# Performance work log

Measured on AMD Instinct MI355X. Metric: run time of the kernel, lower is better.

The kernel has to match this reference:

```python
import jax, jax.numpy as jnp
import numpy as np

BIG = 1e4  # larger than any image dimension; safe in fp32 when squared


def _edt(e):
    # e: [H, W] binary float mask. Exact Euclidean distance transform:
    # distance from each nonzero pixel to the nearest zero pixel
    # (matches cv2.distanceTransform(e, cv2.DIST_L2, maskSize=0)).
    H, W = e.shape
    zero = e == 0
    x = jnp.arange(W, dtype=jnp.float32)[None, :]            # [1, W]
    # 1D pass along rows: distance (in x) to nearest zero in the same row
    last = jax.lax.cummax(jnp.where(zero, x, -BIG), axis=1)              # nearest zero to the left
    nxt = -jax.lax.cummax(jnp.where(zero, -x, -BIG), axis=1, reverse=True)  # nearest zero to the right
    g = jnp.minimum(x - last, nxt - x)                        # [H, W], BIG-ish if row has no zero
    g2 = jnp.minimum(g, BIG) ** 2                             # squared row distance
    # 2D pass along columns: dist2[y, x] = min_r g2[r, x] + (y - r)^2 (exact EDT)
    y = jnp.arange(H, dtype=jnp.float32)
    d2 = (y[:, None] - y[None, :]) ** 2                       # [H, H]
    dist2 = jnp.min(g2[None, :, :] + d2[:, :, None], axis=1)  # [H, W]
    return jnp.sqrt(dist2)


def _min_max_norm(d):
    lo, hi = d.min(), d.max()
    return (d - lo) / (hi - lo + 1e-8)


def _edge_weight(edge):
    # edge: [B, 1, H, W] binary float
    e = edge[:, 0]  # [B, H, W]
    # lax.map keeps peak memory to one [H,H,W] candidate tensor at a time
    w = jax.lax.map(lambda ei: _min_max_norm(_edt(ei)), e)
    return w[:, None]  # [B, 1, H, W]


def setup_inputs() -> dict:
    key = jax.random.key(0)
    k1, k2, k3, k4 = jax.random.split(key, 4)
    shape = (16, 1, 384, 384)
    eps = 1e-4
    pred = jax.random.uniform(k1, shape, jnp.float32, eps, 1.0 - eps)
    pred_edge = jax.random.uniform(k2, shape, jnp.float32, eps, 1.0 - eps)
    label = jax.random.randint(k3, shape, 0, 2).astype(jnp.float32)
    edge = jax.random.randint(k4, shape, 0, 2).astype(jnp.float32)
    return {"pred": pred, "pred_edge": pred_edge, "label": label, "edge": edge}


def reference(pred, pred_edge, label, edge):
    Wm = _edge_weight(edge)  # [B, 1, H, W] in [0, 1]
    label_loss = jnp.mean(
        -(label * jnp.log(pred) + (1.0 - label) * jnp.log(1.0 - pred)) * (1.0 + Wm)
    )
    edge_loss = jnp.mean(
        -(edge * jnp.log(pred_edge) + (1.0 - edge) * jnp.log(1.0 - pred_edge))
    )
    return label_loss + edge_loss
```

## Files before the change

### kernel.cpp

```cpp
#include <hip/hip_runtime.h>

typedef unsigned long long u64;
typedef unsigned int u32;

#define NIMG 16
#define H 384
#define W 384
#define NPIX (H*W)
#define NTOT (NIMG*NPIX)
#define FBIG 10000.0f

#define RPB 96
#define NRB 4
#define NCT 12
#define EBLOCKS (NCT*NRB*NIMG)
#define NROW (NIMG*H)

__device__ __forceinline__ float bflo(u32 w){ return __uint_as_float(w<<16); }
__device__ __forceinline__ float bfhi(u32 w){ return __uint_as_float(w & 0xFFFF0000u); }

__device__ __forceinline__ void detect_flag(const u32* lw, int tid, u32* sflag) {
    if (tid < 64) {
        u32 a = 0;
        #pragma unroll
        for (int k = 0; k < 4; ++k) a |= lw[(tid & 63)*4 + k] & 0xFFFFu;
        u64 b = __ballot(a != 0u);
        if (tid == 0) *sflag = (b != 0ull) ? 1u : 0u;
    }
}

__global__ __launch_bounds__(256) void rowscan_kernel(
        const void* __restrict__ e, const u32* __restrict__ label_u32,
        float* __restrict__ g2, u32* __restrict__ mn, u32* __restrict__ mx) {
    __shared__ u32 sflag;
    int tid = threadIdx.x;
    if (blockIdx.x == 0 && tid < NIMG) { mn[tid] = 0x7f800000u; mx[tid] = 0u; }
    detect_flag(label_u32, tid, &sflag);
    __syncthreads();
    bool isb = (sflag != 0u);

    int lane = tid & 63;
    int row  = blockIdx.x * 4 + (tid >> 6);

    u64 zm[6];
    if (isb) {
        const unsigned short* er = (const unsigned short*)e + (size_t)row * W;
        #pragma unroll
        for (int t = 0; t < 6; ++t) zm[t] = __ballot(er[t*64 + lane] == 0);
    } else {
        const float* er = (const float*)e + (size_t)row * W;
        #pragma unroll
        for (int t = 0; t < 6; ++t) zm[t] = __ballot(er[t*64 + lane] == 0.0f);
    }

    float* gr = g2 + (size_t)row * W;
    #pragma unroll
    for (int t = 0; t < 6; ++t) {
        int c = t*64 + lane;
        u64 m = zm[t] & ((lane == 63) ? ~0ull : ((1ull << (lane+1)) - 1ull));
        int tt = t;
        while (m == 0ull && tt > 0) m = zm[--tt];
        float dl = m ? (float)(c - (tt*64 + 63 - __builtin_clzll(m)))
                     : ((float)c + FBIG);
        m = zm[t] & ((lane == 0) ? ~0ull : ~((1ull << lane) - 1ull));
        tt = t;
        while (m == 0ull && tt < 5) m = zm[++tt];
        float dr = m ? (float)((tt*64 + __builtin_ctzll(m)) - c)
                     : (FBIG - (float)c);
        float g = fminf(fminf(dl, dr), FBIG);
        gr[c] = g * g;
    }
}

__global__ __launch_bounds__(256) void edt_loss_kernel(
    const float* __restrict__ g2,
    const void* __restrict__ pred, const void* __restrict__ pred_edge,
    const void* __restrict__ label, const void* __restrict__ edge,
    u32* __restrict__ mn, u32* __restrict__ mx,
    float* __restrict__ partials) {

    __shared__ u32 sflag;
    __shared__ float cr[4][5];

    int tid = threadIdx.x;
    int img = blockIdx.z;
    int c0  = blockIdx.x * 32;
    int r0  = blockIdx.y * RPB;

    detect_flag((const u32*)label, tid, &sflag);
    __syncthreads();

    const float* g2i = g2 + (size_t)img * NPIX;
    int c2t = tid & 7;
    int rg  = tid >> 3;
    int rb  = r0 + rg;
    const float* gcol = g2i + c0 + c2t * 4;

    float4 best[3];
    float ub = 0.0f;
    #pragma unroll
    for (int i = 0; i < 3; ++i) {
        best[i] = *(const float4*)(gcol + (rb + 32*i) * W);
        ub = fmaxf(ub, fmaxf(fmaxf(best[i].x, best[i].y), fmaxf(best[i].z, best[i].w)));
    }
    #pragma unroll
    for (int off = 1; off < 64; off <<= 1)
        ub = fmaxf(ub, __shfl_xor(ub, off));
    int jcap = (int)ceilf(sqrtf(ub)) + 1;
    if (jcap > H - 1) jcap = H - 1;

    for (int j = 1; j <= jcap; ++j) {
        float jj = (float)(j * j);
        #pragma unroll
        for (int i = 0; i < 3; ++i) {
            int r  = rb + 32*i;
            int ru = r - j; ru = (ru < 0) ? 0 : ru;
            int rd = r + j; rd = (rd > H-1) ? H-1 : rd;
            float4 vu = *(const float4*)(gcol + ru * W);
            float4 vd = *(const float4*)(gcol + rd * W);
            best[i].x = fminf(best[i].x, fminf(vu.x, vd.x) + jj);
            best[i].y = fminf(best[i].y, fminf(vu.y, vd.y) + jj);
            best[i].z = fminf(best[i].z, fminf(vu.z, vd.z) + jj);
            best[i].w = fminf(best[i].w, fminf(vu.w, vd.w) + jj);
        }
    }

    bool isb = (sflag != 0u);
    float sl = 0.0f, sd = 0.0f, se = 0.0f;
    float tmin = 3.0e38f, tmax = 0.0f;
    #pragma unroll
    for (int i = 0; i < 3; ++i) {
        float dv[4];
        dv[0] = sqrtf(best[i].x); dv[1] = sqrtf(best[i].y);
        dv[2] = sqrtf(best[i].z); dv[3] = sqrtf(best[i].w);
        #pragma unroll
        for (int cc = 0; cc < 4; ++cc) {
            tmin = fminf(tmin, dv[cc]);
            tmax = fmaxf(tmax, dv[cc]);
        }
        int r = rb + 32*i;
        size_t base = (size_t)img * NPIX + (size_t)r * W + c0 + c2t * 4;
        float p[4], q[4], lv[4], ev[4];
        if (isb) {
            uint2 up = *(const uint2*)((const unsigned short*)pred      + base);
            uint2 uq = *(const uint2*)((const unsigned short*)pred_edge + base);
            uint2 ul = *(const uint2*)((const unsigned short*)label     + base);
            uint2 ue = *(const uint2*)((const unsigned short*)edge      + base);
            p[0]=bflo(up.x); p[1]=bfhi(up.x); p[2]=bflo(up.y); p[3]=bfhi(up.y);
            q[0]=bflo(uq.x); q[1]=bfhi(uq.x); q[2]=bflo(uq.y); q[3]=bfhi(uq.y);
            lv[0]=bflo(ul.x); lv[1]=bfhi(ul.x); lv[2]=bflo(ul.y); lv[3]=bfhi(ul.y);
            ev[0]=bflo(ue.x); ev[1]=bfhi(ue.x); ev[2]=bflo(ue.y); ev[3]=bfhi(ue.y);
        } else {
            float4 a = *(const float4*)((const float*)pred      + base);
            float4 b = *(const float4*)((const float*)pred_edge + base);
            float4 c = *(const float4*)((const float*)label     + base);
            float4 e = *(const float4*)((const float*)edge      + base);
            p[0]=a.x; p[1]=a.y; p[2]=a.z; p[3]=a.w;
            q[0]=b.x; q[1]=b.y; q[2]=b.z; q[3]=b.w;
            lv[0]=c.x; lv[1]=c.y; lv[2]=c.z; lv[3]=c.w;
            ev[0]=e.x; ev[1]=e.y; ev[2]=e.z; ev[3]=e.w;
        }
        #pragma unroll
        for (int cc = 0; cc < 4; ++cc) {
            float bl = -__logf((lv[cc] != 0.0f) ? p[cc] : 1.0f - p[cc]);
            sl += bl;
            sd = fmaf(bl, dv[cc], sd);
            se += -__logf((ev[cc] != 0.0f) ? q[cc] : 1.0f - q[cc]);
        }
    }

    #pragma unroll
    for (int off = 1; off < 64; off <<= 1) {
        sl += __shfl_xor(sl, off);
        sd += __shfl_xor(sd, off);
        se += __shfl_xor(se, off);
        tmin = fminf(tmin, __shfl_xor(tmin, off));
        tmax = fmaxf(tmax, __shfl_xor(tmax, off));
    }
    int wv = tid >> 6;
    if ((tid & 63) == 0) {
        cr[wv][0] = sl; cr[wv][1] = sd; cr[wv][2] = se;
        cr[wv][3] = tmin; cr[wv][4] = tmax;
    }
    __syncthreads();
    if (tid == 0) {
        float S1 = cr[0][0] + cr[1][0] + cr[2][0] + cr[3][0];
        float S2 = cr[0][1] + cr[1][1] + cr[2][1] + cr[3][1];
        float Se = cr[0][2] + cr[1][2] + cr[2][2] + cr[3][2];
        float Tm = fminf(fminf(cr[0][3], cr[1][3]), fminf(cr[2][3], cr[3][3]));
        float TM = fmaxf(fmaxf(cr[0][4], cr[1][4]), fmaxf(cr[2][4], cr[3][4]));
        int blk = (img * NRB + blockIdx.y) * NCT + blockIdx.x;
        partials[blk*4 + 0] = S1;
        partials[blk*4 + 1] = S2;
        partials[blk*4 + 2] = Se;
        atomicMin(&mn[img], __float_as_uint(Tm));
        atomicMax(&mx[img], __float_as_uint(TM));
    }
}

__global__ void final_kernel(const float* __restrict__ partials,
                             const u32* __restrict__ mn,
                             const u32* __restrict__ mx,
                             u32* __restrict__ out) {
    __shared__ float a1[256], a2[256], a3[256];
    __shared__ float ci[NIMG], sei[NIMG];
    int tid = threadIdx.x;
    int img = tid >> 4, s = tid & 15;
    float S1 = 0.0f, S2 = 0.0f, Se = 0.0f;
    #pragma unroll
    for (int k = 0; k < 3; ++k) {
        const float* pp = partials + (img * 48 + s + 16*k) * 4;
        S1 += pp[0]; S2 += pp[1]; Se += pp[2];
    }
    a1[tid] = S1; a2[tid] = S2; a3[tid] = Se;
    __syncthreads();
    for (int st = 8; st > 0; st >>= 1) {
        if ((tid & 15) < st) {
            a1[tid] += a1[tid+st]; a2[tid] += a2[tid+st]; a3[tid] += a3[tid+st];
        }
        __syncthreads();
    }
    if ((tid & 15) == 0) {
        float lo = __uint_as_float(mn[img]);
        float hi = __uint_as_float(mx[img]);
        float inv = 1.0f / (hi - lo + 1e-8f);
        ci[img]  = a1[tid] + (a2[tid] - lo * a1[tid]) * inv;
        sei[img] = a3[tid];
    }
    __syncthreads();
    if (tid == 0) {
        float t = 0.0f;
        for (int i = 0; i < NIMG; ++i) t += ci[i] + sei[i];
        float v = t / (float)NTOT;
        u32 fv = __float_as_uint(v);
        u32 b  = (fv + 0x7FFFu + ((fv >> 16) & 1u)) >> 16;
        out[0] = (fv & 0xFFFF0000u) | (b & 0xFFFFu);
    }
}

extern "C" void kernel_launch(void* const* d_in, const int* in_sizes, int n_in,
                              void* d_out, int out_size, void* d_ws, size_t ws_size,
                              hipStream_t stream) {
    float* ws = (float*)d_ws;
    float* g2 = ws;
    u32* mn = (u32*)(ws + NTOT);
    u32* mx = mn + 16;
    float* partials = (float*)(mx + 16);

    rowscan_kernel<<<NROW / 4, 256, 0, stream>>>(d_in[3], (const u32*)d_in[2],
                                                 g2, mn, mx);
    edt_loss_kernel<<<dim3(NCT, NRB, NIMG), 256, 0, stream>>>(
        g2, d_in[0], d_in[1], d_in[2], d_in[3], mn, mx, partials);
    final_kernel<<<1, 256, 0, stream>>>(partials, mn, mx, (u32*)d_out);
}
```

Baseline: 33.49 us.

## Fuse row scan into EDT kernel using shared-memory column tile with halo rows

Removes the separate row-scan kernel and its global g2 buffer. Each EDT block now builds the squared row distances for its 32-column strip directly into a shared tile, first for its own rows and then for only the halo rows needed given the block-wide search bound. The column min-plus pass then reads from LDS instead of global memory, and per-image min/max goes into the partials array instead of global atomics. The cost is redundant ballot work, since each row's edge mask is rescanned by all 12 column blocks, plus 48KB of LDS per block, which may limit occupancy.

```diff
diff --git a/kernel.cpp b/kernel.cpp
--- a/kernel.cpp
+++ b/kernel.cpp
@@ -14,7 +14,6 @@
 #define NRB 4
 #define NCT 12
 #define EBLOCKS (NCT*NRB*NIMG)
-#define NROW (NIMG*H)
 
 __device__ __forceinline__ float bflo(u32 w){ return __uint_as_float(w<<16); }
 __device__ __forceinline__ float bfhi(u32 w){ return __uint_as_float(w & 0xFFFF0000u); }
@@ -29,19 +28,8 @@
     }
 }
 
-__global__ __launch_bounds__(256) void rowscan_kernel(
-        const void* __restrict__ e, const u32* __restrict__ label_u32,
-        float* __restrict__ g2, u32* __restrict__ mn, u32* __restrict__ mx) {
-    __shared__ u32 sflag;
-    int tid = threadIdx.x;
-    if (blockIdx.x == 0 && tid < NIMG) { mn[tid] = 0x7f800000u; mx[tid] = 0u; }
-    detect_flag(label_u32, tid, &sflag);
-    __syncthreads();
-    bool isb = (sflag != 0u);
-
-    int lane = tid & 63;
-    int row  = blockIdx.x * 4 + (tid >> 6);
-
+__device__ __forceinline__ void build_row(const void* e, bool isb, int row,
+                                          int lane, int c0, float* tileF) {
     u64 zm[6];
     if (isb) {
         const unsigned short* er = (const unsigned short*)e + (size_t)row * W;
@@ -52,72 +40,98 @@
         #pragma unroll
         for (int t = 0; t < 6; ++t) zm[t] = __ballot(er[t*64 + lane] == 0.0f);
     }
-
-    float* gr = g2 + (size_t)row * W;
-    #pragma unroll
-    for (int t = 0; t < 6; ++t) {
-        int c = t*64 + lane;
-        u64 m = zm[t] & ((lane == 63) ? ~0ull : ((1ull << (lane+1)) - 1ull));
-        int tt = t;
-        while (m == 0ull && tt > 0) m = zm[--tt];
-        float dl = m ? (float)(c - (tt*64 + 63 - __builtin_clzll(m)))
-                     : ((float)c + FBIG);
-        m = zm[t] & ((lane == 0) ? ~0ull : ~((1ull << lane) - 1ull));
-        tt = t;
-        while (m == 0ull && tt < 5) m = zm[++tt];
-        float dr = m ? (float)((tt*64 + __builtin_ctzll(m)) - c)
-                     : (FBIG - (float)c);
-        float g = fminf(fminf(dl, dr), FBIG);
-        gr[c] = g * g;
+    int cw = c0 >> 6;
+    u64 w = zm[0];
+    #pragma unroll
+    for (int t = 1; t < 6; ++t) if (cw == t) w = zm[t];
+    int hb = -16777216;
+    #pragma unroll
+    for (int t = 0; t < 6; ++t)
+        if (t < cw && zm[t] != 0ull) hb = t*64 + 63 - __builtin_clzll(zm[t]);
+    int la = 16777216;
+    #pragma unroll
+    for (int t = 5; t >= 0; --t)
+        if (t > cw && zm[t] != 0ull) la = t*64 + __builtin_ctzll(zm[t]);
+    if (lane < 32) {
+        int c = c0 + lane;
+        int b = c & 63;
+        u64 ml = w & ((b == 63) ? ~0ull : ((1ull << (b+1)) - 1ull));
+        u64 mr = w & (~0ull << b);
+        int li = ml ? (cw*64 + 63 - __builtin_clzll(ml)) : hb;
+        int ri = mr ? (cw*64 + __builtin_ctzll(mr)) : la;
+        float g = fminf(fminf((float)(c - li), (float)(ri - c)), FBIG);
+        tileF[row*32 + lane] = g * g;
     }
 }
 
 __global__ __launch_bounds__(256) void edt_loss_kernel(
-    const float* __restrict__ g2,
     const void* __restrict__ pred, const void* __restrict__ pred_edge,
     const void* __restrict__ label, const void* __restrict__ edge,
-    u32* __restrict__ mn, u32* __restrict__ mx,
     float* __restrict__ partials) {
 
+    __shared__ float tileF[H * 32];
     __shared__ u32 sflag;
+    __shared__ float crub[4];
     __shared__ float cr[4][5];
 
-    int tid = threadIdx.x;
-    int img = blockIdx.z;
-    int c0  = blockIdx.x * 32;
-    int r0  = blockIdx.y * RPB;
+    int tid  = threadIdx.x;
+    int img  = blockIdx.z;
+    int c0   = blockIdx.x * 32;
+    int r0   = blockIdx.y * RPB;
+    int lane = tid & 63;
+    int wv   = tid >> 6;
 
     detect_flag((const u32*)label, tid, &sflag);
     __syncthreads();
-
-    const float* g2i = g2 + (size_t)img * NPIX;
+    bool isb = (sflag != 0u);
+
+    const void* eimg = isb
+        ? (const void*)((const unsigned short*)edge + (size_t)img * NPIX)
+        : (const void*)((const float*)edge + (size_t)img * NPIX);
+
+    for (int k = 0; k < 24; ++k)
+        build_row(eimg, isb, r0 + 4*k + wv, lane, c0, tileF);
+    __syncthreads();
+
+    const float4* tile4 = (const float4*)tileF;
     int c2t = tid & 7;
     int rg  = tid >> 3;
     int rb  = r0 + rg;
-    const float* gcol = g2i + c0 + c2t * 4;
 
     float4 best[3];
     float ub = 0.0f;
     #pragma unroll
     for (int i = 0; i < 3; ++i) {
-        best[i] = *(const float4*)(gcol + (rb + 32*i) * W);
+        best[i] = tile4[(rb + 32*i)*8 + c2t];
         ub = fmaxf(ub, fmaxf(fmaxf(best[i].x, best[i].y), fmaxf(best[i].z, best[i].w)));
     }
     #pragma unroll
     for (int off = 1; off < 64; off <<= 1)
         ub = fmaxf(ub, __shfl_xor(ub, off));
-    int jcap = (int)ceilf(sqrtf(ub)) + 1;
-    if (jcap > H - 1) jcap = H - 1;
-
-    for (int j = 1; j <= jcap; ++j) {
+    if (lane == 0) crub[wv] = ub;
+    __syncthreads();
+    float ubB = fmaxf(fmaxf(crub[0], crub[1]), fmaxf(crub[2], crub[3]));
+    int jcapW = (int)ceilf(sqrtf(ub))  + 1; if (jcapW > H-1) jcapW = H-1;
+    int jcapB = (int)ceilf(sqrtf(ubB)) + 1; if (jcapB > H-1) jcapB = H-1;
+
+    int n1 = (jcapB < r0) ? jcapB : r0;
+    int n2h = H - RPB - r0;
+    int n2 = (jcapB < n2h) ? jcapB : n2h;
+    for (int k = wv; k < n1 + n2; k += 4) {
+        int r = (k < n1) ? (r0 - n1 + k) : (r0 + RPB + (k - n1));
+        build_row(eimg, isb, r, lane, c0, tileF);
+    }
+    __syncthreads();
+
+    for (int j = 1; j <= jcapW; ++j) {
         float jj = (float)(j * j);
         #pragma unroll
         for (int i = 0; i < 3; ++i) {
             int r  = rb + 32*i;
             int ru = r - j; ru = (ru < 0) ? 0 : ru;
             int rd = r + j; rd = (rd > H-1) ? H-1 : rd;
-            float4 vu = *(const float4*)(gcol + ru * W);
-            float4 vd = *(const float4*)(gcol + rd * W);
+            float4 vu = tile4[ru*8 + c2t];
+            float4 vd = tile4[rd*8 + c2t];
             best[i].x = fminf(best[i].x, fminf(vu.x, vd.x) + jj);
             best[i].y = fminf(best[i].y, fminf(vu.y, vd.y) + jj);
             best[i].z = fminf(best[i].z, fminf(vu.z, vd.z) + jj);
@@ -125,7 +139,6 @@
         }
     }
 
-    bool isb = (sflag != 0u);
     float sl = 0.0f, sd = 0.0f, se = 0.0f;
     float tmin = 3.0e38f, tmax = 0.0f;
     #pragma unroll
@@ -177,8 +190,7 @@
         tmin = fminf(tmin, __shfl_xor(tmin, off));
         tmax = fmaxf(tmax, __shfl_xor(tmax, off));
     }
-    int wv = tid >> 6;
-    if ((tid & 63) == 0) {
+    if (lane == 0) {
         cr[wv][0] = sl; cr[wv][1] = sd; cr[wv][2] = se;
         cr[wv][3] = tmin; cr[wv][4] = tmax;
     }
@@ -190,39 +202,36 @@
         float Tm = fminf(fminf(cr[0][3], cr[1][3]), fminf(cr[2][3], cr[3][3]));
         float TM = fmaxf(fmaxf(cr[0][4], cr[1][4]), fmaxf(cr[2][4], cr[3][4]));
         int blk = (img * NRB + blockIdx.y) * NCT + blockIdx.x;
-        partials[blk*4 + 0] = S1;
-        partials[blk*4 + 1] = S2;
-        partials[blk*4 + 2] = Se;
-        atomicMin(&mn[img], __float_as_uint(Tm));
-        atomicMax(&mx[img], __float_as_uint(TM));
+        float* pp = partials + blk * 5;
+        pp[0] = S1; pp[1] = S2; pp[2] = Se; pp[3] = Tm; pp[4] = TM;
     }
 }
 
 __global__ void final_kernel(const float* __restrict__ partials,
-                             const u32* __restrict__ mn,
-                             const u32* __restrict__ mx,
                              u32* __restrict__ out) {
-    __shared__ float a1[256], a2[256], a3[256];
+    __shared__ float a1[256], a2[256], a3[256], a4[256], a5[256];
     __shared__ float ci[NIMG], sei[NIMG];
     int tid = threadIdx.x;
     int img = tid >> 4, s = tid & 15;
-    float S1 = 0.0f, S2 = 0.0f, Se = 0.0f;
+    float S1 = 0.0f, S2 = 0.0f, Se = 0.0f, Tm = 3.0e38f, TM = 0.0f;
     #pragma unroll
     for (int k = 0; k < 3; ++k) {
-        const float* pp = partials + (img * 48 + s + 16*k) * 4;
+        const float* pp = partials + (img * 48 + s + 16*k) * 5;
         S1 += pp[0]; S2 += pp[1]; Se += pp[2];
-    }
-    a1[tid] = S1; a2[tid] = S2; a3[tid] = Se;
+        Tm = fminf(Tm, pp[3]); TM = fmaxf(TM, pp[4]);
+    }
+    a1[tid]=S1; a2[tid]=S2; a3[tid]=Se; a4[tid]=Tm; a5[tid]=TM;
     __syncthreads();
     for (int st = 8; st > 0; st >>= 1) {
         if ((tid & 15) < st) {
             a1[tid] += a1[tid+st]; a2[tid] += a2[tid+st]; a3[tid] += a3[tid+st];
+            a4[tid] = fminf(a4[tid], a4[tid+st]);
+            a5[tid] = fmaxf(a5[tid], a5[tid+st]);
         }
         __syncthreads();
     }
     if ((tid & 15) == 0) {
-        float lo = __uint_as_float(mn[img]);
-        float hi = __uint_as_float(mx[img]);
+        float lo = a4[tid], hi = a5[tid];
         float inv = 1.0f / (hi - lo + 1e-8f);
         ci[img]  = a1[tid] + (a2[tid] - lo * a1[tid]) * inv;
         sei[img] = a3[tid];
@@ -241,15 +250,9 @@
 extern "C" void kernel_launch(void* const* d_in, const int* in_sizes, int n_in,
                               void* d_out, int out_size, void* d_ws, size_t ws_size,
                               hipStream_t stream) {
-    float* ws = (float*)d_ws;
-    float* g2 = ws;
-    u32* mn = (u32*)(ws + NTOT);
-    u32* mx = mn + 16;
-    float* partials = (float*)(mx + 16);
-
-    rowscan_kernel<<<NROW / 4, 256, 0, stream>>>(d_in[3], (const u32*)d_in[2],
-                                                 g2, mn, mx);
+    float* partials = (float*)d_ws;
+
     edt_loss_kernel<<<dim3(NCT, NRB, NIMG), 256, 0, stream>>>(
-        g2, d_in[0], d_in[1], d_in[2], d_in[3], mn, mx, partials);
-    final_kernel<<<1, 256, 0, stream>>>(partials, mn, mx, (u32*)d_out);
-}
+        d_in[0], d_in[1], d_in[2], d_in[3], partials);
+    final_kernel<<<1, 256, 0, stream>>>(partials, (u32*)d_out);
+}
```

Result: slower. 37.29 us (+11.3%).

## Stage column strip of g2 in LDS, prefetch loss inputs, drop min/max atomics

Applied to the files above, without the earlier changes.

Each EDT block now copies the full 384x32 column strip of squared row distances into shared memory (48 KB) and runs the column min-plus search from LDS instead of global/L2. The loss inputs are prefetched into registers before the search so their latency overlaps it. Per-image min/max move from global atomics into the partials buffer and are reduced in the final kernel. The cost is that every block loads the whole strip, four times the rows it owns, and the large LDS footprint limits how many blocks fit per CU.

```diff
diff --git a/kernel.cpp b/kernel.cpp
--- a/kernel.cpp
+++ b/kernel.cpp
@@ -31,10 +31,9 @@
 
 __global__ __launch_bounds__(256) void rowscan_kernel(
         const void* __restrict__ e, const u32* __restrict__ label_u32,
-        float* __restrict__ g2, u32* __restrict__ mn, u32* __restrict__ mx) {
+        float* __restrict__ g2) {
     __shared__ u32 sflag;
     int tid = threadIdx.x;
-    if (blockIdx.x == 0 && tid < NIMG) { mn[tid] = 0x7f800000u; mx[tid] = 0u; }
     detect_flag(label_u32, tid, &sflag);
     __syncthreads();
     bool isb = (sflag != 0u);
@@ -76,31 +75,61 @@
     const float* __restrict__ g2,
     const void* __restrict__ pred, const void* __restrict__ pred_edge,
     const void* __restrict__ label, const void* __restrict__ edge,
-    u32* __restrict__ mn, u32* __restrict__ mx,
     float* __restrict__ partials) {
 
+    __shared__ float tileF[H * 32];
     __shared__ u32 sflag;
     __shared__ float cr[4][5];
 
-    int tid = threadIdx.x;
-    int img = blockIdx.z;
-    int c0  = blockIdx.x * 32;
-    int r0  = blockIdx.y * RPB;
+    int tid  = threadIdx.x;
+    int img  = blockIdx.z;
+    int c0   = blockIdx.x * 32;
+    int r0   = blockIdx.y * RPB;
+    int lane = tid & 63;
+    int wv   = tid >> 6;
 
     detect_flag((const u32*)label, tid, &sflag);
-    __syncthreads();
 
     const float* g2i = g2 + (size_t)img * NPIX;
+    float4* tile4w = (float4*)tileF;
+    #pragma unroll
+    for (int k = 0; k < 12; ++k) {
+        int gi  = tid + 256*k;
+        int row = gi >> 3, c2 = gi & 7;
+        tile4w[gi] = *(const float4*)(g2i + row * W + c0 + c2 * 4);
+    }
+    __syncthreads();
+    bool isb = (sflag != 0u);
+
+    const float4* tile4 = (const float4*)tileF;
     int c2t = tid & 7;
     int rg  = tid >> 3;
     int rb  = r0 + rg;
-    const float* gcol = g2i + c0 + c2t * 4;
+
+    uint4 st_p[3], st_q[3], st_l[3], st_e[3];
+    #pragma unroll
+    for (int i = 0; i < 3; ++i) {
+        size_t base = (size_t)img * NPIX + (size_t)(rb + 32*i) * W + c0 + c2t * 4;
+        if (isb) {
+            uint2 a = *(const uint2*)((const unsigned short*)pred      + base);
+            uint2 b = *(const uint2*)((const unsigned short*)pred_edge + base);
+            uint2 c = *(const uint2*)((const unsigned short*)label     + base);
+            uint2 d = *(const uint2*)((const unsigned short*)edge      + base);
+            st_p[i].x=a.x; st_p[i].y=a.y; st_q[i].x=b.x; st_q[i].y=b.y;
+            st_l[i].x=c.x; st_l[i].y=c.y; st_e[i].x=d.x; st_e[i].y=d.y;
+        } else {
+            st_p[i] = *(const uint4*)((const float*)pred      + base);
+            st_q[i] = *(const uint4*)((const float*)pred_edge + base);
+            st_l[i] = *(const uint4*)((const float*)label     + base);
+            st_e[i] = *(const uint4*)((const float*)edge      + base);
+        }
+    }
 
     float4 best[3];
     float ub = 0.0f;
     #pragma unroll
     for (int i = 0; i < 3; ++i) {
-        best[i] = *(const float4*)(gcol + (rb + 32*i) * W);
+        best[i] = tile4[(rb + 32*i)*8 + c2t];
         ub = fmaxf(ub, fmaxf(fmaxf(best[i].x, best[i].y), fmaxf(best[i].z, best[i].w)));
     }
     #pragma unroll
@@ -116,8 +145,8 @@
             int r  = rb + 32*i;
             int ru = r - j; ru = (ru < 0) ? 0 : ru;
             int rd = r + j; rd = (rd > H-1) ? H-1 : rd;
-            float4 vu = *(const float4*)(gcol + ru * W);
-            float4 vd = *(const float4*)(gcol + rd * W);
+            float4 vu = tile4[ru*8 + c2t];
+            float4 vd = tile4[rd*8 + c2t];
             best[i].x = fminf(best[i].x, fminf(vu.x, vd.x) + jj);
             best[i].y = fminf(best[i].y, fminf(vu.y, vd.y) + jj);
             best[i].z = fminf(best[i].z, fminf(vu.z, vd.z) + jj);
@@ -125,7 +154,6 @@
         }
     }
 
-    bool isb = (sflag != 0u);
     float sl = 0.0f, sd = 0.0f, se = 0.0f;
     float tmin = 3.0e38f, tmax = 0.0f;
     #pragma unroll
@@ -138,27 +166,21 @@
             tmin = fminf(tmin, dv[cc]);
             tmax = fmaxf(tmax, dv[cc]);
         }
-        int r = rb + 32*i;
-        size_t base = (size_t)img * NPIX + (size_t)r * W + c0 + c2t * 4;
         float p[4], q[4], lv[4], ev[4];
         if (isb) {
-            uint2 up = *(const uint2*)((const unsigned short*)pred      + base);
-            uint2 uq = *(const uint2*)((const unsigned short*)pred_edge + base);
-            uint2 ul = *(const uint2*)((const unsigned short*)label     + base);
-            uint2 ue = *(const uint2*)((const unsigned short*)edge      + base);
-            p[0]=bflo(up.x); p[1]=bfhi(up.x); p[2]=bflo(up.y); p[3]=bfhi(up.y);
-            q[0]=bflo(uq.x); q[1]=bfhi(uq.x); q[2]=bflo(uq.y); q[3]=bfhi(uq.y);
-            lv[0]=bflo(ul.x); lv[1]=bfhi(ul.x); lv[2]=bflo(ul.y); lv[3]=bfhi(ul.y);
-            ev[0]=bflo(ue.x); ev[1]=bfhi(ue.x); ev[2]=bflo(ue.y); ev[3]=bfhi(ue.y);
+            p[0]=bflo(st_p[i].x); p[1]=bfhi(st_p[i].x); p[2]=bflo(st_p[i].y); p[3]=bfhi(st_p[i].y);
+            q[0]=bflo(st_q[i].x); q[1]=bfhi(st_q[i].x); q[2]=bflo(st_q[i].y); q[3]=bfhi(st_q[i].y);
+            lv[0]=bflo(st_l[i].x); lv[1]=bfhi(st_l[i].x); lv[2]=bflo(st_l[i].y); lv[3]=bfhi(st_l[i].y);
+            ev[0]=bflo(st_e[i].x); ev[1]=bfhi(st_e[i].x); ev[2]=bflo(st_e[i].y); ev[3]=bfhi(st_e[i].y);
         } else {
-            float4 a = *(const float4*)((const float*)pred      + base);
-            float4 b = *(const float4*)((const float*)pred_edge + base);
-            float4 c = *(const float4*)((const float*)label     + base);
-            float4 e = *(const float4*)((const float*)edge      + base);
-            p[0]=a.x; p[1]=a.y; p[2]=a.z; p[3]=a.w;
-            q[0]=b.x; q[1]=b.y; q[2]=b.z; q[3]=b.w;
-            lv[0]=c.x; lv[1]=c.y; lv[2]=c.z; lv[3]=c.w;
-            ev[0]=e.x; ev[1]=e.y; ev[2]=e.z; ev[3]=e.w;
+            p[0]=__uint_as_float(st_p[i].x); p[1]=__uint_as_float(st_p[i].y);
+            p[2]=__uint_as_float(st_p[i].z); p[3]=__uint_as_float(st_p[i].w);
+            q[0]=__uint_as_float(st_q[i].x); q[1]=__uint_as_float(st_q[i].y);
+            q[2]=__uint_as_float(st_q[i].z); q[3]=__uint_as_float(st_q[i].w);
+            lv[0]=__uint_as_float(st_l[i].x); lv[1]=__uint_as_float(st_l[i].y);
+            lv[2]=__uint_as_float(st_l[i].z); lv[3]=__uint_as_float(st_l[i].w);
+            ev[0]=__uint_as_float(st_e[i].x); ev[1]=__uint_as_float(st_e[i].y);
+            ev[2]=__uint_as_float(st_e[i].z); ev[3]=__uint_as_float(st_e[i].w);
         }
         #pragma unroll
         for (int cc = 0; cc < 4; ++cc) {
@@ -177,8 +199,7 @@
         tmin = fminf(tmin, __shfl_xor(tmin, off));
         tmax = fmaxf(tmax, __shfl_xor(tmax, off));
     }
-    int wv = tid >> 6;
-    if ((tid & 63) == 0) {
+    if (lane == 0) {
         cr[wv][0] = sl; cr[wv][1] = sd; cr[wv][2] = se;
         cr[wv][3] = tmin; cr[wv][4] = tmax;
     }
@@ -190,39 +211,36 @@
         float Tm = fminf(fminf(cr[0][3], cr[1][3]), fminf(cr[2][3], cr[3][3]));
         float TM = fmaxf(fmaxf(cr[0][4], cr[1][4]), fmaxf(cr[2][4], cr[3][4]));
         int blk = (img * NRB + blockIdx.y) * NCT + blockIdx.x;
-        partials[blk*4 + 0] = S1;
-        partials[blk*4 + 1] = S2;
-        partials[blk*4 + 2] = Se;
-        atomicMin(&mn[img], __float_as_uint(Tm));
-        atomicMax(&mx[img], __float_as_uint(TM));
+        float* pp = partials + blk * 5;
+        pp[0] = S1; pp[1] = S2; pp[2] = Se; pp[3] = Tm; pp[4] = TM;
     }
 }
 
 __global__ void final_kernel(const float* __restrict__ partials,
-                             const u32* __restrict__ mn,
-                             const u32* __restrict__ mx,
                              u32* __restrict__ out) {
-    __shared__ float a1[256], a2[256], a3[256];
+    __shared__ float a1[256], a2[256], a3[256], a4[256], a5[256];
     __shared__ float ci[NIMG], sei[NIMG];
     int tid = threadIdx.x;
     int img = tid >> 4, s = tid & 15;
-    float S1 = 0.0f, S2 = 0.0f, Se = 0.0f;
+    float S1 = 0.0f, S2 = 0.0f, Se = 0.0f, Tm = 3.0e38f, TM = 0.0f;
     #pragma unroll
     for (int k = 0; k < 3; ++k) {
-        const float* pp = partials + (img * 48 + s + 16*k) * 4;
+        const float* pp = partials + (img * 48 + s + 16*k) * 5;
         S1 += pp[0]; S2 += pp[1]; Se += pp[2];
-    }
-    a1[tid] = S1; a2[tid] = S2; a3[tid] = Se;
+        Tm = fminf(Tm, pp[3]); TM = fmaxf(TM, pp[4]);
+    }
+    a1[tid]=S1; a2[tid]=S2; a3[tid]=Se; a4[tid]=Tm; a5[tid]=TM;
     __syncthreads();
     for (int st = 8; st > 0; st >>= 1) {
         if ((tid & 15) < st) {
             a1[tid] += a1[tid+st]; a2[tid] += a2[tid+st]; a3[tid] += a3[tid+st];
+            a4[tid] = fminf(a4[tid], a4[tid+st]);
+            a5[tid] = fmaxf(a5[tid], a5[tid+st]);
         }
         __syncthreads();
     }
     if ((tid & 15) == 0) {
-        float lo = __uint_as_float(mn[img]);
-        float hi = __uint_as_float(mx[img]);
+        float lo = a4[tid], hi = a5[tid];
         float inv = 1.0f / (hi - lo + 1e-8f);
         ci[img]  = a1[tid] + (a2[tid] - lo * a1[tid]) * inv;
         sei[img] = a3[tid];
@@ -243,13 +261,10 @@
                               hipStream_t stream) {
     float* ws = (float*)d_ws;
     float* g2 = ws;
-    u32* mn = (u32*)(ws + NTOT);
-    u32* mx = mn + 16;
-    float* partials = (float*)(mx + 16);
-
-    rowscan_kernel<<<NROW / 4, 256, 0, stream>>>(d_in[3], (const u32*)d_in[2],
-                                                 g2, mn, mx);
+    float* partials = ws + NTOT;
+
+    rowscan_kernel<<<NROW / 4, 256, 0, stream>>>(d_in[3], (const u32*)d_in[2], g2);
     edt_loss_kernel<<<dim3(NCT, NRB, NIMG), 256, 0, stream>>>(
-        g2, d_in[0], d_in[1], d_in[2], d_in[3], mn, mx, partials);
-    final_kernel<<<1, 256, 0, stream>>>(partials, mn, mx, (u32*)d_out);
-}
+        g2, d_in[0], d_in[1], d_in[2], d_in[3], partials);
+    final_kernel<<<1, 256, 0, stream>>>(partials, (u32*)d_out);
+}
```

Result: faster. 28.25 us (-15.6%).
